# Optimization experiments

Measured on AMD Instinct MI355X. Metric: run time of the kernel, lower is better.

## Reference

```python
import jax, jax.numpy as jnp
import numpy as np

BATCH, SEQ_LEN, ENC_IN = 16, 1024, 12
N_HIPPO, MODES, OUT_DIM = 256, 32, 5
MULTISCALE = [1, 2, 4]
EPS_VAR, EPS_AFF = 1e-5, 1e-10


def _transition_lmu(N):
    Q = np.arange(N, dtype=np.float64)
    R = (2 * Q + 1)[:, None]
    j, i = np.meshgrid(Q, Q)
    A = np.where(i < j, -1.0, (-1.0) ** (i - j + 1)) * R
    B = (-1.0) ** Q[:, None] * R
    return A, B


def _bilinear_discretize(A, B, dt):
    # scipy.signal.cont2discrete(..., method='bilinear')
    N = A.shape[0]
    I = np.eye(N)
    ima = I - (dt / 2.0) * A
    Ad = np.linalg.solve(ima, I + (dt / 2.0) * A)
    Bd = np.linalg.solve(ima, dt * B)
    return Ad, Bd.squeeze(-1)


def _eval_legendre(N, x):
    # P_n(x) for n=0..N-1 via three-term recurrence; returns (len(x), N)
    P = np.zeros((len(x), N), dtype=np.float64)
    P[:, 0] = 1.0
    if N > 1:
        P[:, 1] = x
    for n in range(1, N - 1):
        P[:, n + 1] = ((2 * n + 1) * x * P[:, n] - n * P[:, n - 1]) / (n + 1)
    return P


def setup_inputs() -> dict:
    key = jax.random.key(0)
    ks = jax.random.split(key, 8)
    A_list, B_list, E_list = [], [], []
    for mult in MULTISCALE:
        dt = 1.0 / SEQ_LEN / mult
        A, B = _transition_lmu(N_HIPPO)
        Ad, Bd = _bilinear_discretize(A, B, dt)
        vals = np.arange(0.0, 1.0, dt)
        ev = _eval_legendre(N_HIPPO, 1.0 - 2.0 * vals)  # (seq_len*mult, N)
        A_list.append(Ad); B_list.append(Bd); E_list.append(ev[-SEQ_LEN:, :])
    scale = 1.0 / (N_HIPPO * N_HIPPO)
    inp = {
        "x_enc": jax.random.normal(ks[0], (BATCH, SEQ_LEN, ENC_IN), jnp.float32),
        "affine_w": jnp.ones((1, 1, ENC_IN), jnp.float32),
        "affine_b": jnp.zeros((1, 1, ENC_IN), jnp.float32),
        "w_spec_re": scale * jax.random.uniform(ks[1], (len(MULTISCALE), N_HIPPO, N_HIPPO, MODES), jnp.float32),
        "w_spec_im": scale * jax.random.uniform(ks[2], (len(MULTISCALE), N_HIPPO, N_HIPPO, MODES), jnp.float32),
        "w_mlp": 0.3 * jax.random.normal(ks[3], (1, len(MULTISCALE)), jnp.float32),
        "b_mlp": jnp.zeros((1,), jnp.float32),
        "w_fc": 0.05 * jax.random.normal(ks[4], (OUT_DIM, ENC_IN), jnp.float32),
        "b_fc": jnp.zeros((OUT_DIM,), jnp.float32),
        "A_mats": jnp.asarray(np.stack(A_list), jnp.float32),   # (3, N, N)
        "B_vecs": jnp.asarray(np.stack(B_list), jnp.float32),   # (3, N)
        "eval_last": jnp.asarray(np.stack(E_list), jnp.float32),  # (3, seq_len, N)
    }
    return inp


def reference(x_enc, affine_w, affine_b, w_spec_re, w_spec_im, w_mlp, b_mlp,
              w_fc, b_fc, A_mats, B_vecs, eval_last):
    L = x_enc.shape[1]
    # RevIN-style normalization (means/stdev are detached in torch)
    means = jax.lax.stop_gradient(jnp.mean(x_enc, axis=1, keepdims=True))
    xc = x_enc - means
    stdev = jax.lax.stop_gradient(jnp.sqrt(jnp.var(xc, axis=1, keepdims=True) + EPS_VAR))
    x = xc / stdev * affine_w + affine_b          # (B, L, C)
    xt = jnp.transpose(x, (0, 2, 1))              # (B, C, L)
    xt_seq = jnp.moveaxis(xt, -1, 0)              # (L, B, C)
    w_spec = (w_spec_re + 1j * w_spec_im).astype(jnp.complex64)
    modes2 = w_spec.shape[-1]
    decs = []
    for s in range(len(MULTISCALE)):
        A, Bv = A_mats[s], B_vecs[s]
        def step(c, f):  # c: (B,C,N), f: (B,C)
            c = c @ A.T + f[..., None] * Bv
            return c, c
        c0 = jnp.zeros(xt.shape[:2] + (A.shape[0],), xt.dtype)
        _, cs = jax.lax.scan(step, c0, xt_seq)    # (L, B, C, N)
        x_in_c = jnp.transpose(cs, (1, 2, 3, 0))  # (B, C, N, L)
        x_ft = jnp.fft.rfft(x_in_c)               # (B, C, N, L//2+1)
        out_low = jnp.einsum('bjix,iox->bjox', x_ft[..., :modes2], w_spec[s])
        out_ft = jnp.pad(out_low, ((0, 0), (0, 0), (0, 0), (0, x_ft.shape[-1] - modes2)))
        out = jnp.fft.irfft(out_ft, n=L)          # (B, C, N, L)
        x_dec_c = out[..., L - 1]                 # (B, C, N)
        decs.append(x_dec_c @ eval_last[s].T)     # (B, C, L)
    xd = jnp.stack(decs, axis=-1)                 # (B, C, L, 3)
    xd = (xd @ w_mlp.T + b_mlp)[..., 0]           # (B, C, L)
    x_dec = jnp.transpose(xd, (0, 2, 1))          # (B, L, C)
    x_dec = (x_dec - affine_b) / (affine_w + EPS_AFF) * stdev + means
    feat = jnp.mean(jnp.transpose(x_dec, (0, 2, 1)), axis=-1)  # (B, C)
    return feat @ w_fc.T + b_fc                   # (B, OUT_DIM)
```

## Files before the change

kernel.cpp:

```cpp
#include <hip/hip_runtime.h>
#include <math.h>

#define LSEQ 1024
#define NB 16
#define NC 12
#define NH 256
#define NM 32
#define NS 3
#define TWO_PI 6.283185307179586f

#define NPL   8
#define PSTR  196608
#define VPSTR 786432

#define OFF_MEANS 0
#define OFF_STDEV 192
#define OFF_EPART 384
#define OFF_WT_RE 24960
#define OFF_WT_IM 49536
#define OFF_VP    74112
#define OFF_V     6365568
#define OFF_PP0   7152000
#define OFF_PP1   8724864
#define OFF_H     10297728

__device__ __forceinline__ float block_reduce_sum(float v, float* sbuf) {
  int t = threadIdx.x;
  sbuf[t] = v; __syncthreads();
  for (int off = 128; off > 0; off >>= 1) {
    if (t < off) sbuf[t] += sbuf[t + off];
    __syncthreads();
  }
  float r = sbuf[0];
  __syncthreads();
  return r;
}

__device__ __forceinline__ void wtilde_task(int w, float* smem,
                                            const float* __restrict__ wre,
                                            const float* __restrict__ wim,
                                            const float* __restrict__ epart,
                                            float* __restrict__ wt_re,
                                            float* __restrict__ wt_im) {
  int s = w >> 8, i = w & 255;
  int t = threadIdx.x;
  float* ebs = smem;
  float* sr  = smem + 256;
  float* si2 = smem + 1280;
  float eb = 0.f;
  for (int ch = 0; ch < 32; ++ch) eb += epart[(s * 32 + ch) * 256 + t];
  ebs[t] = eb * (1.0f / LSEQ);
  __syncthreads();
  const float* br = wre + (size_t)(s * NH + i) * NH * NM;
  const float* bi = wim + (size_t)(s * NH + i) * NH * NM;
  float aR[4] = {0.f, 0.f, 0.f, 0.f}, aI[4] = {0.f, 0.f, 0.f, 0.f};
  #pragma unroll
  for (int it = 0; it < 8; ++it) {
    int o = (t >> 3) + 32 * it;
    float e = ebs[o];
    float4 vr = *(const float4*)(br + (size_t)t * 4 + 1024 * it);
    float4 vi = *(const float4*)(bi + (size_t)t * 4 + 1024 * it);
    aR[0] += e * vr.x; aR[1] += e * vr.y; aR[2] += e * vr.z; aR[3] += e * vr.w;
    aI[0] += e * vi.x; aI[1] += e * vi.y; aI[2] += e * vi.z; aI[3] += e * vi.w;
  }
  *(float4*)(sr + t * 4)  = make_float4(aR[0], aR[1], aR[2], aR[3]);
  *(float4*)(si2 + t * 4) = make_float4(aI[0], aI[1], aI[2], aI[3]);
  __syncthreads();
  if (t < 32) {
    float r = 0.f, im = 0.f;
    #pragma unroll
    for (int og = 0; og < 32; ++og) { r += sr[og * 32 + t]; im += si2[og * 32 + t]; }
    wt_re[(size_t)(s * NM + t) * NH + i] = r;
    wt_im[(size_t)(s * NM + t) * NH + i] = im;
  }
  __syncthreads();
}

#define FMA_ROW(r, av) { acc[r][0] += (av)*b4.x; acc[r][1] += (av)*b4.y; acc[r][2] += (av)*b4.z; acc[r][3] += (av)*b4.w; }

template<int ANP, int BNP>
__device__ __forceinline__ void gemm32(float* As, float* Bs,
                       const float* Abase, int apstr,
                       const float* Bbase, int bpstr, int bld, int colLimit,
                       int rowbase, int colbase, int kb,
                       float* outp, int outld, int outcol0, int outColLim) {
  const int tid = threadIdx.x;
  const int tx = tid & 15, ty = tid >> 4;
  const int kkA = tid & 31, rA = tid >> 5;
  const int jB = tid & 63, kB = tid >> 6;
  float acc[8][4];
  #pragma unroll
  for (int i = 0; i < 8; ++i)
    #pragma unroll
    for (int j = 0; j < 4; ++j) acc[i][j] = 0.f;

  #pragma unroll
  for (int p = 0; p < 16; ++p) {
    int row = rowbase + rA + 8 * p;
    float pv[ANP];
    #pragma unroll
    for (int pp = 0; pp < ANP; ++pp)
      pv[pp] = Abase[(size_t)pp * apstr + (size_t)row * 256 + kb + kkA];
    float v = pv[0];
    #pragma unroll
    for (int pp = 1; pp < ANP; ++pp) v += pv[pp];
    As[kkA * 132 + rA + 8 * p] = v;
  }
  #pragma unroll
  for (int q = 0; q < 8; ++q) {
    int kk = kB + 4 * q;
    int j = colbase + jB;
    float v = 0.f;
    if (j < colLimit) {
      float pv[BNP];
      #pragma unroll
      for (int pp = 0; pp < BNP; ++pp)
        pv[pp] = Bbase[(size_t)pp * bpstr + (size_t)(kb + kk) * bld + j];
      v = pv[0];
      #pragma unroll
      for (int pp = 1; pp < BNP; ++pp) v += pv[pp];
    }
    Bs[kk * 68 + jB] = v;
  }
  __syncthreads();
  #pragma unroll
  for (int kk = 0; kk < 32; ++kk) {
    float4 b4 = *(const float4*)(Bs + kk * 68 + tx * 4);
    float4 a0 = *(const float4*)(As + kk * 132 + ty * 8);
    float4 a1 = *(const float4*)(As + kk * 132 + ty * 8 + 4);
    FMA_ROW(0, a0.x) FMA_ROW(1, a0.y) FMA_ROW(2, a0.z) FMA_ROW(3, a0.w)
    FMA_ROW(4, a1.x) FMA_ROW(5, a1.y) FMA_ROW(6, a1.z) FMA_ROW(7, a1.w)
  }
  __syncthreads();
  if (colbase + 64 <= outColLim) {
    #pragma unroll
    for (int i = 0; i < 8; ++i) {
      int row = rowbase + ty * 8 + i;
      float4 st; st.x = acc[i][0]; st.y = acc[i][1]; st.z = acc[i][2]; st.w = acc[i][3];
      *(float4*)(outp + (size_t)row * outld + outcol0 + colbase + tx * 4) = st;
    }
  } else {
    #pragma unroll
    for (int i = 0; i < 8; ++i) {
      int row = rowbase + ty * 8 + i;
      #pragma unroll
      for (int j = 0; j < 4; ++j) {
        int c = colbase + tx * 4 + j;
        if (c < outColLim) outp[(size_t)row * outld + outcol0 + c] = acc[i][j];
      }
    }
  }
}

template<int ANP>
__global__ __launch_bounds__(256) void k_chain(const float* __restrict__ Pc,
                                               float* __restrict__ Pn,
                                               float* __restrict__ Vp,
                                               int m, int nSq, int ntct,
                                               const float* __restrict__ wre,
                                               const float* __restrict__ wim,
                                               const float* __restrict__ epart_c,
                                               float* __restrict__ wt_re,
                                               float* __restrict__ wt_im,
                                               int wstart, int wcount,
                                               const float* __restrict__ x,
                                               float* __restrict__ means,
                                               float* __restrict__ stdev,
                                               int statCount, int redCount,
                                               float* __restrict__ V,
                                               const float* __restrict__ ev,
                                               float* __restrict__ epart_w,
                                               int epCount,
                                               const float* __restrict__ Bv,
                                               int v01Count,
                                               const float* __restrict__ b_fc,
                                               float* __restrict__ H,
                                               float* __restrict__ out,
                                               int hCount) {
  __shared__ float smem[6608];
  float* As = smem;
  float* Bs = smem + 4224;
  const int blk = blockIdx.x;
  const int t = threadIdx.x;
  const int nExt = 48 * ntct;
  const int b0 = nSq + nExt;
  const int b1 = b0 + wcount;
  const int b2 = b1 + statCount;
  const int b3 = b2 + redCount;
  const int b4_ = b3 + epCount;
  const int b5 = b4_ + v01Count;
  if (blk < nSq) {
    int slice = blk & 7, rest = blk >> 3;
    int t8 = rest & 7, s = rest >> 3;
    int rt = t8 & 1, ct = t8 >> 1;
    const float* Ab = Pc + (size_t)s * 65536;
    gemm32<ANP, ANP>(As, Bs, Ab, PSTR, Ab, PSTR, 256, 256,
           rt * 128, ct * 64, slice * 32,
           Pn + (size_t)slice * PSTR + (size_t)s * 65536, 256, 0, 256);
  } else if (blk < b0) {
    int e = blk - nSq;
    int slice = e & 7, rt = (e >> 3) & 1, rest2 = e >> 4;
    int ct = rest2 % ntct, s = rest2 / ntct;
    gemm32<ANP, NPL>(As, Bs, Pc + (size_t)s * 65536, PSTR,
           Vp + (size_t)s * 262144, VPSTR, 1024, m,
           rt * 128, ct * 64, slice * 32,
           Vp + (size_t)slice * VPSTR + (size_t)s * 262144, 1024, m, m);
  } else if (blk < b1) {
    wtilde_task(wstart + (blk - b0), smem, wre, wim, epart_c, wt_re, wt_im);
  } else if (blk < b2) {
    int bc = blk - b1;
    int b = bc / NC, c = bc % NC;
    float* xs = smem;
    float* red = smem + 1024;
    for (int e = 0; e < 4; ++e) {
      int tau = t + 256 * e;
      xs[tau] = x[((size_t)b * LSEQ + tau) * NC + c];
    }
    __syncthreads();
    float p = 0.f;
    for (int e = 0; e < 4; ++e) p += xs[t + 256 * e];
    float sum = block_reduce_sum(p, red);
    float mean = sum * (1.0f / LSEQ);
    float q = 0.f;
    for (int e = 0; e < 4; ++e) { float d = xs[t + 256 * e] - mean; q += d * d; }
    float sq = block_reduce_sum(q, red);
    if (t == 0) {
      means[bc] = mean;
      stdev[bc] = sqrtf(sq * (1.0f / LSEQ) + 1e-5f);
    }
  } else if (blk < b3) {
    int rid = blk - b2;
    for (int e = 0; e < 2; ++e) {
      size_t idx = (size_t)rid * 1024 + e * 256 + t;
      float v = 0.f;
      #pragma unroll
      for (int pl = 0; pl < NPL; ++pl) v += Vp[(size_t)pl * VPSTR + idx];
      V[idx] = v;
    }
  } else if (blk < b4_) {
    int bb = blk - b3;
    int s = bb >> 5, ch = bb & 31;
    float acc = 0.f;
    const float* base = ev + (size_t)s * LSEQ * NH + (size_t)ch * 32 * NH + t;
    for (int l = 0; l < 32; ++l) acc += base[(size_t)l * NH];
    epart_w[(size_t)bb * NH + t] = acc;
  } else if (blk < b5) {
    int v = blk - b4_;
    int s = v >> 1, half = v & 1;
    float* bsh = smem;
    float* psh = smem + 256;
    bsh[t] = Bv[s * 256 + t];
    __syncthreads();
    int i = half * 128 + (t >> 1);
    int k2 = (t & 1) * 128;
    const float* Arow = Pc + (size_t)s * 65536 + (size_t)i * 256 + k2;
    float acc = 0.f;
    for (int kk = 0; kk < 128; ++kk) acc += Arow[kk] * bsh[k2 + kk];
    psh[t] = acc;
    __syncthreads();
    if ((t & 1) == 0) {
      int row = s * 256 + i;
      Vp[(size_t)row * 1024 + 1] = psh[t] + psh[t + 1];
      Vp[(size_t)row * 1024] = bsh[i];
    }
    for (int z = t; z < 7 * 128 * 2; z += 256) {
      int pl = 1 + (z >> 8);
      int rr2 = (z >> 1) & 127;
      int col = z & 1;
      int row = s * 256 + half * 128 + rr2;
      Vp[(size_t)pl * VPSTR + (size_t)row * 1024 + col] = 0.f;
    }
  } else if (blk < b5 + hCount) {
    for (int e = 0; e < 4; ++e) H[t + 256 * e] = 0.0f;
    if (t < NB * 5) out[t] = b_fc[t % 5];
  }
}

__global__ __launch_bounds__(256) void k_reduceV2(const float* __restrict__ Vp,
                                                  float* __restrict__ V) {
  int t = threadIdx.x;
  for (int e = 0; e < 2; ++e) {
    size_t idx = (size_t)blockIdx.x * 1024 + 512 + e * 256 + t;
    float v = 0.f;
    #pragma unroll
    for (int pl = 0; pl < NPL; ++pl) v += Vp[(size_t)pl * VPSTR + idx];
    V[idx] = v;
  }
}

__global__ __launch_bounds__(256) void k_utscan(const float* __restrict__ wt_re,
                                                const float* __restrict__ wt_im,
                                                const float* __restrict__ V,
                                                const float* __restrict__ w_mlp,
                                                float* __restrict__ H) {
  int blk = blockIdx.x;
  int s = blk / NM, k = blk & 31;
  int t = threadIdx.x;
  __shared__ float sr[LSEQ], si_[LSEQ];
  __shared__ float cr[256], ci[256];
  const float* wr = wt_re + (size_t)blk * NH;
  const float* wi_ = wt_im + (size_t)blk * NH;
  const float* Vs = V + (size_t)s * NH * LSEQ;
  float ar[4] = {0.f, 0.f, 0.f, 0.f}, ai[4] = {0.f, 0.f, 0.f, 0.f};
  for (int i = 0; i < NH; ++i) {
    float a = wr[i], b = wi_[i];
    float4 v4 = *(const float4*)(Vs + (size_t)i * LSEQ + 4 * t);
    ar[0] += a * v4.x; ai[0] += b * v4.x;
    ar[1] += a * v4.y; ai[1] += b * v4.y;
    ar[2] += a * v4.z; ai[2] += b * v4.z;
    ar[3] += a * v4.w; ai[3] += b * v4.w;
  }
  float lr[4], li[4], rr = 0.f, ii = 0.f;
  #pragma unroll
  for (int e = 0; e < 4; ++e) {
    int d = 4 * t + e;
    int frac = (k * d) & 1023;
    float ang = -(TWO_PI / 1024.0f) * (float)frac;
    float sn, csn; sincosf(ang, &sn, &csn);
    float tr = ar[e] * csn - ai[e] * sn;
    float ti = ar[e] * sn + ai[e] * csn;
    rr += tr; ii += ti;
    lr[e] = rr; li[e] = ii;
  }
  cr[t] = rr; ci[t] = ii;
  __syncthreads();
  for (int off = 1; off < 256; off <<= 1) {
    float pr = 0.f, pi = 0.f;
    if (t >= off) { pr = cr[t - off]; pi = ci[t - off]; }
    __syncthreads();
    cr[t] += pr; ci[t] += pi;
    __syncthreads();
  }
  float offr = (t > 0) ? cr[t - 1] : 0.0f;
  float offi = (t > 0) ? ci[t - 1] : 0.0f;
  #pragma unroll
  for (int e = 0; e < 4; ++e) {
    sr[4 * t + e] = lr[e] + offr;
    si_[4 * t + e] = li[e] + offi;
  }
  __syncthreads();
  float wm = w_mlp[s];
  float coef = wm * ((k == 0) ? 1.0f : 2.0f) * (1.0f / LSEQ);
  for (int e = 0; e < 4; ++e) {
    int tau = t + 256 * e;
    int mIdx = 1023 - tau;
    int frac = (k * (tau + 1)) & 1023;
    float ang = -(TWO_PI / 1024.0f) * (float)frac;
    float sn, csn; sincosf(ang, &sn, &csn);
    float val = coef * (sr[mIdx] * csn - si_[mIdx] * sn);
    atomicAdd(&H[tau], val);
  }
}

__global__ __launch_bounds__(256) void k_feat(const float* __restrict__ x,
                                              const float* __restrict__ means,
                                              const float* __restrict__ stdev,
                                              const float* __restrict__ aw,
                                              const float* __restrict__ ab,
                                              const float* __restrict__ b_mlp,
                                              const float* __restrict__ H,
                                              const float* __restrict__ w_fc,
                                              float* __restrict__ out) {
  int bc = blockIdx.x; int b = bc / NC, c = bc % NC;
  __shared__ float red[256];
  int t = threadIdx.x;
  float mn = means[bc], sd = stdev[bc];
  float w = aw[c], bb = ab[c];
  float acc = 0.f;
  for (int e = 0; e < 4; ++e) {
    int tau = t + 256 * e;
    float xv = x[((size_t)b * LSEQ + tau) * NC + c];
    float f = (xv - mn) / sd * w + bb;
    acc += f * H[tau];
  }
  float sum = block_reduce_sum(acc, red);
  if (t == 0) {
    float mr = sum + b_mlp[0];
    float featv = (mr - bb) / (w + 1e-10f) * sd + mn;
    #pragma unroll
    for (int d = 0; d < 5; ++d)
      atomicAdd(&out[b * 5 + d], featv * w_fc[d * NC + c]);
  }
}

extern "C" void kernel_launch(void* const* d_in, const int* in_sizes, int n_in,
                              void* d_out, int out_size, void* d_ws, size_t ws_size,
                              hipStream_t stream) {
  const float* x_enc   = (const float*)d_in[0];
  const float* aw      = (const float*)d_in[1];
  const float* ab      = (const float*)d_in[2];
  const float* wre     = (const float*)d_in[3];
  const float* wim     = (const float*)d_in[4];
  const float* w_mlp   = (const float*)d_in[5];
  const float* b_mlp   = (const float*)d_in[6];
  const float* w_fc    = (const float*)d_in[7];
  const float* b_fc    = (const float*)d_in[8];
  const float* A_mats  = (const float*)d_in[9];
  const float* B_vecs  = (const float*)d_in[10];
  const float* ev      = (const float*)d_in[11];

  float* ws    = (float*)d_ws;
  float* means = ws + OFF_MEANS;
  float* stdev = ws + OFF_STDEV;
  float* epart = ws + OFF_EPART;
  float* wt_re = ws + OFF_WT_RE;
  float* wt_im = ws + OFF_WT_IM;
  float* Vp    = ws + OFF_VP;
  float* V     = ws + OFF_V;
  float* PP0   = ws + OFF_PP0;
  float* PP1   = ws + OFF_PP1;
  float* H     = ws + OFF_H;
  float* out   = (float*)d_out;

  static const int wcn[5] = {154, 154, 154, 154, 152};
  static const int wst[5] = {0, 154, 308, 462, 616};
  const float* Pc = A_mats;
  float* Pn = PP0;
  for (int si = 0; si < 10; ++si) {
    int m = 1 << si;
    int doSq = (si < 9);
    int nSq = doSq ? 192 : 0;
    int ntct = (si == 0) ? 0 : ((m + 63) >> 6);
    int wstart = (si >= 1 && si <= 5) ? wst[si - 1] : 0;
    int wcount = (si >= 1 && si <= 5) ? wcn[si - 1] : 0;
    int statCount = (si == 0) ? 192 : 0;
    int redCount = (si == 9) ? 768 : 0;
    int epCount = (si == 0) ? 96 : 0;
    int v01Count = (si == 0) ? 6 : 0;
    int hCount = (si == 0) ? 1 : 0;
    int grid = nSq + 48 * ntct + wcount + statCount + redCount + epCount + v01Count + hCount;
    if (si == 0)
      k_chain<1><<<grid, 256, 0, stream>>>(Pc, Pn, Vp, m, nSq, ntct,
          wre, wim, epart, wt_re, wt_im, wstart, wcount,
          x_enc, means, stdev, statCount, redCount, V,
          ev, epart, epCount, B_vecs, v01Count, b_fc, H, out, hCount);
    else
      k_chain<NPL><<<grid, 256, 0, stream>>>(Pc, Pn, Vp, m, nSq, ntct,
          wre, wim, epart, wt_re, wt_im, wstart, wcount,
          x_enc, means, stdev, statCount, redCount, V,
          ev, epart, epCount, B_vecs, v01Count, b_fc, H, out, hCount);
    if (doSq) { Pc = Pn; Pn = (Pn == PP0) ? PP1 : PP0; }
  }

  k_reduceV2<<<768, 256, 0, stream>>>(Vp, V);
  k_utscan<<<NS * NM, 256, 0, stream>>>(wt_re, wt_im, V, w_mlp, H);
  k_feat<<<192, 256, 0, stream>>>(x_enc, means, stdev, aw, ab, b_mlp, H, w_fc, out);
}
```

Baseline: 161.2 us.

## Replace final doubling stage with projected weight product and merge V reduction

The tenth chain launch extended V by multiplying the 256x512 V half by the final power matrix. That step is dropped. Instead, a new kernel reduces the partial planes of the last power matrix and multiplies it by the wtilde weights, giving z9 (32x256 per scale), and the scan applies z9 to the first half of V to cover the upper 512 columns. The full V reduction is folded into the same kernel. This removes one launch and a large GEMM, at the cost of an extra small projection GEMM and shared-memory weight staging in the scan.

```diff
diff --git a/kernel.cpp b/kernel.cpp
--- a/kernel.cpp
+++ b/kernel.cpp
@@ -23,6 +23,8 @@
 #define OFF_PP0   7152000
 #define OFF_PP1   8724864
 #define OFF_H     10297728
+#define OFF_Z9R   10298752
+#define OFF_Z9I   10323328
 
 __device__ __forceinline__ float block_reduce_sum(float v, float* sbuf) {
   int t = threadIdx.x;
@@ -166,8 +168,7 @@
                                                const float* __restrict__ x,
                                                float* __restrict__ means,
                                                float* __restrict__ stdev,
-                                               int statCount, int redCount,
-                                               float* __restrict__ V,
+                                               int statCount,
                                                const float* __restrict__ ev,
                                                float* __restrict__ epart_w,
                                                int epCount,
@@ -186,9 +187,8 @@
   const int b0 = nSq + nExt;
   const int b1 = b0 + wcount;
   const int b2 = b1 + statCount;
-  const int b3 = b2 + redCount;
-  const int b4_ = b3 + epCount;
-  const int b5 = b4_ + v01Count;
+  const int b3 = b2 + epCount;
+  const int b4_ = b3 + v01Count;
   if (blk < nSq) {
     int slice = blk & 7, rest = blk >> 3;
     int t8 = rest & 7, s = rest >> 3;
@@ -229,23 +229,14 @@
       stdev[bc] = sqrtf(sq * (1.0f / LSEQ) + 1e-5f);
     }
   } else if (blk < b3) {
-    int rid = blk - b2;
-    for (int e = 0; e < 2; ++e) {
-      size_t idx = (size_t)rid * 1024 + e * 256 + t;
-      float v = 0.f;
-      #pragma unroll
-      for (int pl = 0; pl < NPL; ++pl) v += Vp[(size_t)pl * VPSTR + idx];
-      V[idx] = v;
-    }
-  } else if (blk < b4_) {
-    int bb = blk - b3;
+    int bb = blk - b2;
     int s = bb >> 5, ch = bb & 31;
     float acc = 0.f;
     const float* base = ev + (size_t)s * LSEQ * NH + (size_t)ch * 32 * NH + t;
     for (int l = 0; l < 32; ++l) acc += base[(size_t)l * NH];
     epart_w[(size_t)bb * NH + t] = acc;
-  } else if (blk < b5) {
-    int v = blk - b4_;
+  } else if (blk < b4_) {
+    int v = blk - b3;
     int s = v >> 1, half = v & 1;
     float* bsh = smem;
     float* psh = smem + 256;
@@ -270,26 +261,79 @@
       int row = s * 256 + half * 128 + rr2;
       Vp[(size_t)pl * VPSTR + (size_t)row * 1024 + col] = 0.f;
     }
-  } else if (blk < b5 + hCount) {
+  } else if (blk < b4_ + hCount) {
     for (int e = 0; e < 4; ++e) H[t + 256 * e] = 0.0f;
     if (t < NB * 5) out[t] = b_fc[t % 5];
   }
 }
 
-__global__ __launch_bounds__(256) void k_reduceV2(const float* __restrict__ Vp,
-                                                  float* __restrict__ V) {
-  int t = threadIdx.x;
-  for (int e = 0; e < 2; ++e) {
-    size_t idx = (size_t)blockIdx.x * 1024 + 512 + e * 256 + t;
-    float v = 0.f;
-    #pragma unroll
-    for (int pl = 0; pl < NPL; ++pl) v += Vp[(size_t)pl * VPSTR + idx];
-    V[idx] = v;
+__global__ __launch_bounds__(256) void k_z9red(const float* __restrict__ Vp,
+                                               float* __restrict__ V,
+                                               const float* __restrict__ Q9,
+                                               const float* __restrict__ wt_re,
+                                               const float* __restrict__ wt_im,
+                                               float* __restrict__ z9r,
+                                               float* __restrict__ z9i) {
+  __shared__ float smem[8448];
+  const int blk = blockIdx.x;
+  const int t = threadIdx.x;
+  if (blk < 768) {
+    for (int e = 0; e < 2; ++e) {
+      size_t idx = (size_t)blk * 1024 + e * 256 + t;
+      float v = 0.f;
+      #pragma unroll
+      for (int pl = 0; pl < NPL; ++pl) v += Vp[(size_t)pl * VPSTR + idx];
+      V[idx] = v;
+    }
+    return;
+  }
+  int zid = blk - 768;
+  int s = zid >> 2, ct = zid & 3;
+  float* Bs2 = smem;
+  float* Asr = smem + 4352;
+  float* Asi = smem + 6400;
+  const float* Qs = Q9 + (size_t)s * 65536;
+  const int k = t & 31, cg = t >> 5;
+  float accR[8], accI[8];
+  #pragma unroll
+  for (int j = 0; j < 8; ++j) { accR[j] = 0.f; accI[j] = 0.f; }
+  for (int kb = 0; kb < 256; kb += 64) {
+    for (int z = t; z < 4096; z += 256) {
+      int row = z >> 6, col = z & 63;
+      float v = 0.f;
+      #pragma unroll
+      for (int pp = 0; pp < NPL; ++pp)
+        v += Qs[(size_t)pp * PSTR + (size_t)(kb + row) * 256 + ct * 64 + col];
+      Bs2[row * 68 + col] = v;
+    }
+    for (int z = t; z < 2048; z += 256) {
+      int k2 = z & 31, kk = z >> 5;
+      Asr[k2 * 64 + kk] = wt_re[(size_t)(s * 32 + k2) * 256 + kb + kk];
+      Asi[k2 * 64 + kk] = wt_im[(size_t)(s * 32 + k2) * 256 + kb + kk];
+    }
+    __syncthreads();
+    for (int kk = 0; kk < 64; ++kk) {
+      float ar_ = Asr[k * 64 + kk], ai_ = Asi[k * 64 + kk];
+      #pragma unroll
+      for (int j = 0; j < 8; ++j) {
+        float b = Bs2[kk * 68 + cg * 8 + j];
+        accR[j] += ar_ * b; accI[j] += ai_ * b;
+      }
+    }
+    __syncthreads();
+  }
+  #pragma unroll
+  for (int j = 0; j < 8; ++j) {
+    size_t o = (size_t)(s * 32 + k) * 256 + ct * 64 + cg * 8 + j;
+    z9r[o] = accR[j];
+    z9i[o] = accI[j];
   }
 }
 
 __global__ __launch_bounds__(256) void k_utscan(const float* __restrict__ wt_re,
                                                 const float* __restrict__ wt_im,
+                                                const float* __restrict__ z9r,
+                                                const float* __restrict__ z9i,
                                                 const float* __restrict__ V,
                                                 const float* __restrict__ w_mlp,
                                                 float* __restrict__ H) {
@@ -298,13 +342,20 @@
   int t = threadIdx.x;
   __shared__ float sr[LSEQ], si_[LSEQ];
   __shared__ float cr[256], ci[256];
-  const float* wr = wt_re + (size_t)blk * NH;
-  const float* wi_ = wt_im + (size_t)blk * NH;
+  __shared__ float wsm[1024];
+  wsm[t]        = wt_re[(size_t)blk * NH + t];
+  wsm[256 + t]  = z9r[(size_t)blk * NH + t];
+  wsm[512 + t]  = wt_im[(size_t)blk * NH + t];
+  wsm[768 + t]  = z9i[(size_t)blk * NH + t];
+  __syncthreads();
   const float* Vs = V + (size_t)s * NH * LSEQ;
+  const int off = (t >> 7) << 8;
+  const int col4 = (4 * t) & 511;
   float ar[4] = {0.f, 0.f, 0.f, 0.f}, ai[4] = {0.f, 0.f, 0.f, 0.f};
   for (int i = 0; i < NH; ++i) {
-    float a = wr[i], b = wi_[i];
-    float4 v4 = *(const float4*)(Vs + (size_t)i * LSEQ + 4 * t);
+    float a = wsm[off + i];
+    float b = wsm[512 + off + i];
+    float4 v4 = *(const float4*)(Vs + (size_t)i * LSEQ + col4);
     ar[0] += a * v4.x; ai[0] += b * v4.x;
     ar[1] += a * v4.y; ai[1] += b * v4.y;
     ar[2] += a * v4.z; ai[2] += b * v4.z;
@@ -324,9 +375,9 @@
   }
   cr[t] = rr; ci[t] = ii;
   __syncthreads();
-  for (int off = 1; off < 256; off <<= 1) {
+  for (int off2 = 1; off2 < 256; off2 <<= 1) {
     float pr = 0.f, pi = 0.f;
-    if (t >= off) { pr = cr[t - off]; pi = ci[t - off]; }
+    if (t >= off2) { pr = cr[t - off2]; pi = ci[t - off2]; }
     __syncthreads();
     cr[t] += pr; ci[t] += pi;
     __syncthreads();
@@ -410,39 +461,39 @@
   float* PP0   = ws + OFF_PP0;
   float* PP1   = ws + OFF_PP1;
   float* H     = ws + OFF_H;
+  float* z9r   = ws + OFF_Z9R;
+  float* z9i   = ws + OFF_Z9I;
   float* out   = (float*)d_out;
 
   static const int wcn[5] = {154, 154, 154, 154, 152};
   static const int wst[5] = {0, 154, 308, 462, 616};
   const float* Pc = A_mats;
   float* Pn = PP0;
-  for (int si = 0; si < 10; ++si) {
+  for (int si = 0; si < 9; ++si) {
     int m = 1 << si;
-    int doSq = (si < 9);
-    int nSq = doSq ? 192 : 0;
+    int nSq = 192;
     int ntct = (si == 0) ? 0 : ((m + 63) >> 6);
     int wstart = (si >= 1 && si <= 5) ? wst[si - 1] : 0;
     int wcount = (si >= 1 && si <= 5) ? wcn[si - 1] : 0;
     int statCount = (si == 0) ? 192 : 0;
-    int redCount = (si == 9) ? 768 : 0;
     int epCount = (si == 0) ? 96 : 0;
     int v01Count = (si == 0) ? 6 : 0;
     int hCount = (si == 0) ? 1 : 0;
-    int grid = nSq + 48 * ntct + wcount + statCount + redCount + epCount + v01Count + hCount;
+    int grid = nSq + 48 * ntct + wcount + statCount + epCount + v01Count + hCount;
     if (si == 0)
       k_chain<1><<<grid, 256, 0, stream>>>(Pc, Pn, Vp, m, nSq, ntct,
           wre, wim, epart, wt_re, wt_im, wstart, wcount,
-          x_enc, means, stdev, statCount, redCount, V,
+          x_enc, means, stdev, statCount,
           ev, epart, epCount, B_vecs, v01Count, b_fc, H, out, hCount);
     else
       k_chain<NPL><<<grid, 256, 0, stream>>>(Pc, Pn, Vp, m, nSq, ntct,
           wre, wim, epart, wt_re, wt_im, wstart, wcount,
-          x_enc, means, stdev, statCount, redCount, V,
+          x_enc, means, stdev, statCount,
           ev, epart, epCount, B_vecs, v01Count, b_fc, H, out, hCount);
-    if (doSq) { Pc = Pn; Pn = (Pn == PP0) ? PP1 : PP0; }
-  }
-
-  k_reduceV2<<<768, 256, 0, stream>>>(Vp, V);
-  k_utscan<<<NS * NM, 256, 0, stream>>>(wt_re, wt_im, V, w_mlp, H);
+    Pc = Pn; Pn = (Pn == PP0) ? PP1 : PP0;
+  }
+
+  k_z9red<<<780, 256, 0, stream>>>(Vp, V, Pc, wt_re, wt_im, z9r, z9i);
+  k_utscan<<<NS * NM, 256, 0, stream>>>(wt_re, wt_im, z9r, z9i, V, w_mlp, H);
   k_feat<<<192, 256, 0, stream>>>(x_enc, means, stdev, aw, ab, b_mlp, H, w_fc, out);
 }
```

Result: slower. 186.3 us (+15.6%).
